# Performance work log

Hardware: AMD Instinct MI355X
Metric: run time of the kernel (lower is better)

## Reference

```python
import jax, jax.numpy as jnp
import numpy as np

DIM = 256
HALF = DIM // 2
B, S = 32, 4096
U_MAX = 4096          # upper bound on number of unique tree positions (positions < S)
MAX_DEPTH = 13        # bitlen(S) covers all path lengths for positions <= S


def setup_inputs() -> dict:
    key = jax.random.key(0)
    k1, k2, k3, k4, k5 = jax.random.split(key, 5)
    token_types = jax.random.randint(k1, (B, S), 0, 5, dtype=jnp.int32)
    node_positions = jax.random.randint(k2, (B, S), 0, S, dtype=jnp.int32)
    small_vals = jax.random.randint(k3, (B, S), 0, 4, dtype=jnp.int32)
    # deBruijn tokens (type 4) reference tree positions -> values must lie in unique(node_positions)
    token_values = jnp.where(token_types == 4, node_positions,
                   jnp.where(token_types == 3, -1, small_vals)).astype(jnp.int32)
    primitives = jax.random.normal(k4, (2, HALF, HALF), dtype=jnp.float32)
    identity = jnp.ones((1, HALF), dtype=jnp.float32)
    embed_weight = jax.random.normal(k5, (11, HALF), dtype=jnp.float32)
    return {"token_types": token_types, "token_values": token_values,
            "node_positions": node_positions, "primitives": primitives,
            "identity": identity, "embed_weight": embed_weight}


def cayley(X):
    # torch orthogonal(..., orthogonal_map='cayley'): A = tril(X) - tril(X)^T (skew), Q = (I - A/2)^{-1}(I + A/2)
    A = jnp.tril(X)
    A = A - jnp.swapaxes(A, -1, -2)
    I = jnp.eye(X.shape[-1], dtype=X.dtype)
    return jnp.linalg.solve(I - 0.5 * A, I + 0.5 * A)


def _forward(token_types, token_values, node_positions, primitives, identity, embed_weight):
    Q = cayley(primitives)                                   # [2, h, h] orthogonal maps
    flat_pos = node_positions.ravel()
    uniq, inv = jnp.unique(flat_pos, return_inverse=True, size=U_MAX, fill_value=S)
    inv = inv.ravel()

    # binary path of pos: bit d of pos for d < bitlen(pos)-1, padded with 2 (pos<=1 -> empty path)
    d = jnp.arange(MAX_DEPTH, dtype=uniq.dtype)
    bits = (uniq[:, None] >> d) & 1                           # [U, D]
    valid = (uniq[:, None] >> (d + 1)) > 0
    word = jnp.where(valid, bits, 2)                          # [U, D]

    maps0 = jnp.broadcast_to(identity, (U_MAX, HALF)).astype(primitives.dtype)

    def step(maps, b):                                        # maps [U, h], b [U]
        m0 = maps @ Q[0].T                                    # linear(maps, primitives[0])
        m1 = maps @ Q[1].T
        maps = jnp.where((b == 0)[:, None], m0,
                jnp.where((b == 1)[:, None], m1, maps))
        return maps, None

    path_emb, _ = jax.lax.scan(step, maps0, word.T)           # [U, h]

    pos_enc = path_emb[inv].reshape(B, S, HALF)               # positional encodings

    sos = token_types == 0
    bop = token_types == 1
    nop = token_types == 2
    oos = (token_types == 3) & (token_values == -1)
    db = token_types == 4

    emb_idx = jnp.where(bop, token_values + 1,
              jnp.where(nop, token_values + 5, 0))
    type_emb = embed_weight[emb_idx]                          # [B, S, h]

    db_idx = jnp.searchsorted(uniq, jnp.clip(token_values, 0, S - 1))  # bucketize into unique positions
    db_emb = path_emb[db_idx]                                 # [B, S, h]

    content = jnp.zeros_like(pos_enc)
    content = jnp.where(sos[..., None], embed_weight[0], content)
    content = jnp.where((bop | nop)[..., None], type_emb, content)
    content = jnp.where(db[..., None], db_emb, content)
    content = jnp.where(oos[..., None], embed_weight[10], content)

    return jnp.concatenate([content, pos_enc], axis=-1)       # [B, S, DIM]


def reference(token_types, token_values, node_positions, primitives, identity, embed_weight):
    return _forward(token_types, token_values, node_positions, primitives, identity, embed_weight)
```

## Files before the change

### kernel.cpp

```cpp
#include <hip/hip_runtime.h>

#define HALF 128
#define NMAT 16384
#define NTOK 131072

__global__ __launch_bounds__(512) void cayley_qt(const float* __restrict__ prim,
                                                 float* __restrict__ QT) {
    __shared__ __align__(16) float Xs[128 * 129];
    __shared__ __align__(16) float CpT[2][16][132];
    __shared__ __align__(16) float Rp [2][16][128];
    __shared__ __align__(16) float Dcol[2][16][20];

    const int b = blockIdx.x;
    const float* __restrict__ X = prim + b * NMAT;
    const int t  = threadIdx.x;
    const int c  = t & 127;
    const int q  = t >> 7;
    const int r0 = q << 5;

    for (int idx4 = t; idx4 < 4096; idx4 += 512) {
        int gi = idx4 << 2;
        float4 v = *(const float4*)(X + gi);
        int r = gi >> 7, cc = gi & 127;
        float* p = &Xs[r * 129 + cc];
        p[0] = v.x; p[1] = v.y; p[2] = v.z; p[3] = v.w;
    }
    __syncthreads();

    float reg[32];
    #pragma unroll
    for (int i = 0; i < 32; ++i) {
        int r  = r0 + i;
        int mx = r > c ? r : c;
        int mn = r ^ c ^ mx;
        float x = Xs[mx * 129 + mn];
        reg[i] = (r == c) ? 1.0f : (r > c ? 0.5f * x : -0.5f * x);
    }

    #pragma unroll
    for (int s = 0; s < 8; ++s) {
        const int  p     = s & 1;
        const int  k0    = s << 4;
        const int  q0    = s >> 1;
        const int  kl    = (s & 1) << 4;
        const bool panel = (c >= k0) && (c < k0 + 16);

        if (panel) {
            const int m = c - k0;
            #pragma unroll
            for (int i = 0; i < 32; i += 4)
                *(float4*)&CpT[p][m][r0 + i] =
                    make_float4(reg[i], reg[i+1], reg[i+2], reg[i+3]);
        }
        if (q == q0) {
            #pragma unroll
            for (int j = 0; j < 16; ++j) Rp[p][j][c] = reg[kl + j];
        }
        __syncthreads();

        if (t < 64) {
            const int cp = t & 15, q4 = t >> 4;
            float dd[4];
            #pragma unroll
            for (int i = 0; i < 4; ++i) dd[i] = Rp[p][q4 * 4 + i][k0 + cp];
            #pragma unroll
            for (int k = 0; k < 16; ++k) {
                float cv[4];
                #pragma unroll
                for (int i = 0; i < 4; ++i) cv[i] = __shfl(dd[i], (q4 << 4) | k);
                float rv   = __shfl(dd[k & 3], ((k >> 2) << 4) | cp);
                float dkk  = __shfl(rv, k);
                float dinv = 1.0f / dkk;
                float sv   = rv * dinv;
                bool  own  = (cp == k);
                float rf   = own ? dinv : sv;
                #pragma unroll
                for (int i = 0; i < 4; ++i)
                    dd[i] = own ? (-dd[i] * dinv) : fmaf(-cv[i], sv, dd[i]);
                dd[k & 3] = (q4 == (k >> 2)) ? rf : dd[k & 3];
            }
            #pragma unroll
            for (int i = 0; i < 4; ++i) Dcol[p][cp][q4 * 4 + i] = dd[i];
        }
        __syncthreads();

        float coeff[16];
        if (!panel) {
            #pragma unroll
            for (int j = 0; j < 16; ++j) coeff[j] = 0.0f;
            #pragma unroll
            for (int j = 0; j < 16; ++j) {
                float rpj = Rp[p][j][c];
                #pragma unroll
                for (int mq = 0; mq < 16; mq += 4) {
                    float4 dv = *(const float4*)&Dcol[p][j][mq];
                    coeff[mq+0] = fmaf(dv.x, rpj, coeff[mq+0]);
                    coeff[mq+1] = fmaf(dv.y, rpj, coeff[mq+1]);
                    coeff[mq+2] = fmaf(dv.z, rpj, coeff[mq+2]);
                    coeff[mq+3] = fmaf(dv.w, rpj, coeff[mq+3]);
                }
            }
        } else {
            const int mp = c - k0;
            #pragma unroll
            for (int j = 0; j < 16; ++j) coeff[j] = Dcol[p][mp][j];
            #pragma unroll
            for (int i = 0; i < 32; ++i) reg[i] = 0.0f;
        }

        #pragma unroll
        for (int m = 0; m < 16; ++m) {
            float cm = coeff[m];
            #pragma unroll
            for (int i = 0; i < 32; i += 4) {
                float4 c4 = *(const float4*)&CpT[p][m][r0 + i];
                reg[i+0] = fmaf(-c4.x, cm, reg[i+0]);
                reg[i+1] = fmaf(-c4.y, cm, reg[i+1]);
                reg[i+2] = fmaf(-c4.z, cm, reg[i+2]);
                reg[i+3] = fmaf(-c4.w, cm, reg[i+3]);
            }
        }
        if (q == q0) {
            #pragma unroll
            for (int j = 0; j < 16; ++j) reg[kl + j] = coeff[j];
        }
    }

    float* __restrict__ out = QT + b * NMAT;
    #pragma unroll
    for (int i = 0; i < 32; ++i) {
        int r = r0 + i;
        out[r * HALF + c] = 2.0f * reg[i] - (r == c ? 1.0f : 0.0f);
    }
}

__global__ __launch_bounds__(256) void path_steps(const float* __restrict__ QT,
                                                  const float* __restrict__ ident,
                                                  float* __restrict__ P,
                                                  int vbase, int d0) {
    __shared__ float vs[2][8][HALF];
    const int t    = threadIdx.x;
    const int rg   = t >> 5;
    const int jj   = (t & 31) << 2;
    const int v    = vbase + (blockIdx.x << 3) + rg;
    const int vmax = vbase + (blockIdx.x << 3) + 7;

    float4 sv;
    if (d0 == 0) {
        sv = *(const float4*)&ident[jj];
    } else {
        const int u = (v & 127) | 128;
        sv = *(const float4*)&P[u * HALF + jj];
    }
    *(float4*)&vs[0][rg][jj] = sv;
    __syncthreads();

    int cur = 0;
    for (int d = d0; d < 13; ++d) {
        if ((vmax >> (d + 1)) == 0) break;
        const bool valid = (v >> (d + 1)) > 0;
        const float* __restrict__ Qm = QT + (((v >> d) & 1) ? NMAT : 0);
        float4 acc = make_float4(0.f, 0.f, 0.f, 0.f);
        #pragma unroll 4
        for (int cc = 0; cc < 128; cc += 4) {
            float4 v4 = *(const float4*)&vs[cur][rg][cc];
            float4 q0 = *(const float4*)&Qm[(cc+0)*HALF + jj];
            float4 q1 = *(const float4*)&Qm[(cc+1)*HALF + jj];
            float4 q2 = *(const float4*)&Qm[(cc+2)*HALF + jj];
            float4 q3 = *(const float4*)&Qm[(cc+3)*HALF + jj];
            acc.x = fmaf(v4.x,q0.x, fmaf(v4.y,q1.x, fmaf(v4.z,q2.x, fmaf(v4.w,q3.x, acc.x))));
            acc.y = fmaf(v4.x,q0.y, fmaf(v4.y,q1.y, fmaf(v4.z,q2.y, fmaf(v4.w,q3.y, acc.y))));
            acc.z = fmaf(v4.x,q0.z, fmaf(v4.y,q1.z, fmaf(v4.z,q2.z, fmaf(v4.w,q3.z, acc.z))));
            acc.w = fmaf(v4.x,q0.w, fmaf(v4.y,q1.w, fmaf(v4.z,q2.w, fmaf(v4.w,q3.w, acc.w))));
        }
        if (!valid) acc = *(const float4*)&vs[cur][rg][jj];
        *(float4*)&vs[cur ^ 1][rg][jj] = acc;
        __syncthreads();
        cur ^= 1;
    }
    *(float4*)&P[v * HALF + jj] = *(const float4*)&vs[cur][rg][jj];
}

__global__ __launch_bounds__(256) void emit_out(const int* __restrict__ tt,
                                                const int* __restrict__ tv,
                                                const int* __restrict__ np,
                                                const float* __restrict__ P,
                                                const float* __restrict__ emb,
                                                float* __restrict__ out) {
    const int i  = (blockIdx.x << 2) + (threadIdx.x >> 6);
    const int jj = (threadIdx.x & 63) << 2;
    const int ty = tt[i];
    const int v  = tv[i];
    float4 val;
    if (jj < 128) {
        if (ty == 0)      val = *(const float4*)&emb[jj];
        else if (ty == 1) val = *(const float4*)&emb[(v + 1) * HALF + jj];
        else if (ty == 2) val = *(const float4*)&emb[(v + 5) * HALF + jj];
        else if (ty == 4) {
            int vc = v < 0 ? 0 : (v > 4095 ? 4095 : v);
            val = *(const float4*)&P[vc * HALF + jj];
        } else val = (v == -1) ? *(const float4*)&emb[10 * HALF + jj]
                               : make_float4(0.f, 0.f, 0.f, 0.f);
    } else {
        const int p = np[i];
        val = *(const float4*)&P[p * HALF + (jj - 128)];
    }
    *(float4*)&out[i * 256 + jj] = val;
}

extern "C" void kernel_launch(void* const* d_in, const int* in_sizes, int n_in,
                              void* d_out, int out_size, void* d_ws, size_t ws_size,
                              hipStream_t stream) {
    const int*   token_types = (const int*)  d_in[0];
    const int*   token_vals  = (const int*)  d_in[1];
    const int*   node_pos    = (const int*)  d_in[2];
    const float* prim        = (const float*)d_in[3];
    const float* ident       = (const float*)d_in[4];
    const float* emb         = (const float*)d_in[5];
    float* out = (float*)d_out;

    float* QT = (float*)d_ws;
    float* P  = (float*)((char*)d_ws + 262144);

    cayley_qt  <<<2,   512, 0, stream>>>(prim, QT);
    path_steps <<<32,  256, 0, stream>>>(QT, ident, P, 0,   0);
    path_steps <<<480, 256, 0, stream>>>(QT, ident, P, 256, 7);
    emit_out   <<<NTOK / 4, 256, 0, stream>>>(token_types, token_vals, node_pos,
                                              P, emb, out);
}
```

Before: 298.8 us.

## Redundant per-wave panel inversion, branchless emit loads, nontemporal output stores

In the Cayley solve, every wavefront now inverts the 16x16 panel block redundantly with 16-wide shuffles and writes its own copy to shared memory. This removes the single-wave inversion stage and one block-wide barrier per step. The step loop is no longer unrolled, and register-half selection uses explicit branches instead of dynamic indexing. The emit kernel computes one source pointer with a single load and writes output with nontemporal stores to reduce cache pollution. The cost is extra redundant ALU and shuffle work and possibly higher register pressure in the Cayley kernel.

```diff
diff --git a/kernel.cpp b/kernel.cpp
--- a/kernel.cpp
+++ b/kernel.cpp
@@ -9,7 +9,7 @@
     __shared__ __align__(16) float Xs[128 * 129];
     __shared__ __align__(16) float CpT[2][16][132];
     __shared__ __align__(16) float Rp [2][16][128];
-    __shared__ __align__(16) float Dcol[2][16][20];
+    __shared__ __align__(16) float Dw [8][16][20];
 
     const int b = blockIdx.x;
     const float* __restrict__ X = prim + b * NMAT;
@@ -17,6 +17,8 @@
     const int c  = t & 127;
     const int q  = t >> 7;
     const int r0 = q << 5;
+    const int w  = t >> 6;
+    const int cp = t & 15;
 
     for (int idx4 = t; idx4 < 4096; idx4 += 512) {
         int gi = idx4 << 2;
@@ -37,12 +39,12 @@
         reg[i] = (r == c) ? 1.0f : (r > c ? 0.5f * x : -0.5f * x);
     }
 
-    #pragma unroll
+    #pragma unroll 1
     for (int s = 0; s < 8; ++s) {
         const int  p     = s & 1;
         const int  k0    = s << 4;
         const int  q0    = s >> 1;
-        const int  kl    = (s & 1) << 4;
+        const bool lo    = (s & 1) == 0;
         const bool panel = (c >= k0) && (c < k0 + 16);
 
         if (panel) {
@@ -53,47 +55,54 @@
                     make_float4(reg[i], reg[i+1], reg[i+2], reg[i+3]);
         }
         if (q == q0) {
-            #pragma unroll
-            for (int j = 0; j < 16; ++j) Rp[p][j][c] = reg[kl + j];
+            if (lo) {
+                #pragma unroll
+                for (int j = 0; j < 16; ++j) Rp[p][j][c] = reg[j];
+            } else {
+                #pragma unroll
+                for (int j = 0; j < 16; ++j) Rp[p][j][c] = reg[16 + j];
+            }
         }
         __syncthreads();
 
-        if (t < 64) {
-            const int cp = t & 15, q4 = t >> 4;
-            float dd[4];
-            #pragma unroll
-            for (int i = 0; i < 4; ++i) dd[i] = Rp[p][q4 * 4 + i][k0 + cp];
-            #pragma unroll
-            for (int k = 0; k < 16; ++k) {
-                float cv[4];
-                #pragma unroll
-                for (int i = 0; i < 4; ++i) cv[i] = __shfl(dd[i], (q4 << 4) | k);
-                float rv   = __shfl(dd[k & 3], ((k >> 2) << 4) | cp);
-                float dkk  = __shfl(rv, k);
-                float dinv = 1.0f / dkk;
-                float sv   = rv * dinv;
-                bool  own  = (cp == k);
-                float rf   = own ? dinv : sv;
-                #pragma unroll
-                for (int i = 0; i < 4; ++i)
-                    dd[i] = own ? (-dd[i] * dinv) : fmaf(-cv[i], sv, dd[i]);
-                dd[k & 3] = (q4 == (k >> 2)) ? rf : dd[k & 3];
-            }
-            #pragma unroll
-            for (int i = 0; i < 4; ++i) Dcol[p][cp][q4 * 4 + i] = dd[i];
-        }
-        __syncthreads();
+        float dd[16];
+        #pragma unroll
+        for (int j = 0; j < 16; ++j) dd[j] = Rp[p][j][k0 + cp];
+        #pragma unroll
+        for (int k = 0; k < 16; ++k) {
+            float dkk  = __shfl(dd[k], k);
+            float dinv = 1.0f / dkk;
+            float cv[16];
+            #pragma unroll
+            for (int i = 0; i < 16; ++i) cv[i] = __shfl(dd[i], k);
+            const bool own = (cp == k);
+            const float sv = dd[k] * dinv;
+            #pragma unroll
+            for (int i = 0; i < 16; ++i) {
+                float nv = own ? (-dd[i] * dinv) : fmaf(-cv[i], sv, dd[i]);
+                dd[i] = (i == k) ? (own ? dinv : sv) : nv;
+            }
+        }
+        if ((t & 63) < 16) {
+            *(float4*)&Dw[w][cp][0]  = make_float4(dd[0], dd[1], dd[2], dd[3]);
+            *(float4*)&Dw[w][cp][4]  = make_float4(dd[4], dd[5], dd[6], dd[7]);
+            *(float4*)&Dw[w][cp][8]  = make_float4(dd[8], dd[9], dd[10], dd[11]);
+            *(float4*)&Dw[w][cp][12] = make_float4(dd[12], dd[13], dd[14], dd[15]);
+        }
 
         float coeff[16];
         if (!panel) {
+            float rr[16];
+            #pragma unroll
+            for (int j = 0; j < 16; ++j) rr[j] = Rp[p][j][c];
             #pragma unroll
             for (int j = 0; j < 16; ++j) coeff[j] = 0.0f;
             #pragma unroll
             for (int j = 0; j < 16; ++j) {
-                float rpj = Rp[p][j][c];
+                float rpj = rr[j];
                 #pragma unroll
                 for (int mq = 0; mq < 16; mq += 4) {
-                    float4 dv = *(const float4*)&Dcol[p][j][mq];
+                    float4 dv = *(const float4*)&Dw[w][j][mq];
                     coeff[mq+0] = fmaf(dv.x, rpj, coeff[mq+0]);
                     coeff[mq+1] = fmaf(dv.y, rpj, coeff[mq+1]);
                     coeff[mq+2] = fmaf(dv.z, rpj, coeff[mq+2]);
@@ -101,9 +110,8 @@
                 }
             }
         } else {
-            const int mp = c - k0;
-            #pragma unroll
-            for (int j = 0; j < 16; ++j) coeff[j] = Dcol[p][mp][j];
+            #pragma unroll
+            for (int j = 0; j < 16; ++j) coeff[j] = dd[j];
             #pragma unroll
             for (int i = 0; i < 32; ++i) reg[i] = 0.0f;
         }
@@ -121,8 +129,13 @@
             }
         }
         if (q == q0) {
-            #pragma unroll
-            for (int j = 0; j < 16; ++j) reg[kl + j] = coeff[j];
+            if (lo) {
+                #pragma unroll
+                for (int j = 0; j < 16; ++j) reg[j] = coeff[j];
+            } else {
+                #pragma unroll
+                for (int j = 0; j < 16; ++j) reg[16 + j] = coeff[j];
+            }
         }
     }
 
@@ -189,23 +202,30 @@
                                                 float* __restrict__ out) {
     const int i  = (blockIdx.x << 2) + (threadIdx.x >> 6);
     const int jj = (threadIdx.x & 63) << 2;
-    const int ty = tt[i];
-    const int v  = tv[i];
     float4 val;
     if (jj < 128) {
-        if (ty == 0)      val = *(const float4*)&emb[jj];
-        else if (ty == 1) val = *(const float4*)&emb[(v + 1) * HALF + jj];
-        else if (ty == 2) val = *(const float4*)&emb[(v + 5) * HALF + jj];
+        const int ty = tt[i], v = tv[i];
+        const float* src;
+        bool zero = false;
+        if (ty == 0)      src = emb + jj;
+        else if (ty == 1) src = emb + (v + 1) * HALF + jj;
+        else if (ty == 2) src = emb + (v + 5) * HALF + jj;
         else if (ty == 4) {
             int vc = v < 0 ? 0 : (v > 4095 ? 4095 : v);
-            val = *(const float4*)&P[vc * HALF + jj];
-        } else val = (v == -1) ? *(const float4*)&emb[10 * HALF + jj]
-                               : make_float4(0.f, 0.f, 0.f, 0.f);
+            src = P + vc * HALF + jj;
+        } else {
+            src = emb + 10 * HALF + jj;
+            zero = (v != -1);
+        }
+        val = *(const float4*)src;
+        if (zero) val = make_float4(0.f, 0.f, 0.f, 0.f);
     } else {
-        const int p = np[i];
-        val = *(const float4*)&P[p * HALF + (jj - 128)];
-    }
-    *(float4*)&out[i * 256 + jj] = val;
+        val = *(const float4*)&P[np[i] * HALF + (jj - 128)];
+    }
+    __builtin_nontemporal_store(val.x, &out[i * 256 + jj + 0]);
+    __builtin_nontemporal_store(val.y, &out[i * 256 + jj + 1]);
+    __builtin_nontemporal_store(val.z, &out[i * 256 + jj + 2]);
+    __builtin_nontemporal_store(val.w, &out[i * 256 + jj + 3]);
 }
 
 extern "C" void kernel_launch(void* const* d_in, const int* in_sizes, int n_in,
```

Result: slower. 327.1 us (+9.5%).
